# Kernel tuning notes

Hardware: AMD Instinct MI355X
Metric: run time of the kernel (lower is better)

The kernel has to match this reference:

```python
import jax, jax.numpy as jnp
import numpy as np

B, N, D, H, L = 64, 512, 10, 256, 128  # batch, max_size(nodes), node_dim, hidden, latent
AA, SS, ATOM = 20, 7, 5
K = 2  # conv kernel size
L_KLD = 1e-3


def _lin(k, i, o, s=0.02):
    k1, k2 = jax.random.split(k)
    return jax.random.normal(k1, (i, o), jnp.float32) * s, jax.random.normal(k2, (o,), jnp.float32) * s


def setup_inputs() -> dict:
    key = jax.random.key(0)
    ks = iter(jax.random.split(key, 40))
    nk = lambda: next(ks)
    x = jax.random.normal(nk(), (B, N, D), jnp.float32)
    aa = jax.random.randint(nk(), (B, N), 0, AA + 1).astype(jnp.float32)  # 0 = pad -> ignore_idx
    ss = jax.random.randint(nk(), (B, N), 0, SS + 1).astype(jnp.float32)
    x = x.at[:, :, 0].set(aa).at[:, :, 1].set(ss)
    adj = (jax.random.uniform(nk(), (B, N, N)) < 0.1).astype(jnp.float32)  # sparse binary adjacency
    node_mask = jax.random.randint(nk(), (B, N), 0, 2).astype(bool)
    eps = jax.random.uniform(nk(), (B, N, L), jnp.float32)  # torch.rand_like -> uniform
    W_rel, b_rel = _lin(nk(), D, H)
    W_root, _ = _lin(nk(), D, H)  # lin_root has no bias in DenseSAGEConv
    W_mu, b_mu = _lin(nk(), H, L)
    W_lv, b_lv = _lin(nk(), H, L)
    Wx1, bx1 = _lin(nk(), L, 512); Wx2, bx2 = _lin(nk(), 512, 512); Wx3, bx3 = _lin(nk(), 512, H)
    Wa1, ba1 = _lin(nk(), L, 512); Wa2, ba2 = _lin(nk(), 512, 512); Wa3, ba3 = _lin(nk(), 512, H)
    Wc1 = jax.random.normal(nk(), (256, N, K), jnp.float32) * 0.02; bc1 = jnp.zeros((256,), jnp.float32)
    Wc2 = jax.random.normal(nk(), (N, 256, K), jnp.float32) * 0.02; bc2 = jnp.zeros((N,), jnp.float32)
    W_fcx, b_fcx = _lin(nk(), H, AA * SS)
    W_fca, b_fca = _lin(nk(), H, ATOM)
    W_fcj, b_fcj = _lin(nk(), L - 2 * (K - 1), N)  # cnn out len: 128->127->126
    return dict(x=x, adj=adj, node_mask=node_mask, eps=eps, W_rel=W_rel, b_rel=b_rel, W_root=W_root,
                W_mu=W_mu, b_mu=b_mu, W_lv=W_lv, b_lv=b_lv,
                Wx1=Wx1, bx1=bx1, Wx2=Wx2, bx2=bx2, Wx3=Wx3, bx3=bx3,
                Wa1=Wa1, ba1=ba1, Wa2=Wa2, ba2=ba2, Wa3=Wa3, ba3=ba3,
                Wc1=Wc1, bc1=bc1, Wc2=Wc2, bc2=bc2,
                W_fcx=W_fcx, b_fcx=b_fcx, W_fca=W_fca, b_fca=b_fca, W_fcj=W_fcj, b_fcj=b_fcj)


def reference(x, adj, node_mask, eps, W_rel, b_rel, W_root, W_mu, b_mu, W_lv, b_lv,
              Wx1, bx1, Wx2, bx2, Wx3, bx3, Wa1, ba1, Wa2, ba2, Wa3, ba3,
              Wc1, bc1, Wc2, bc2, W_fcx, b_fcx, W_fca, b_fca, W_fcj, b_fcj):
    relu = jax.nn.relu
    # --- encode: DenseSAGEConv(x, adj, mask) ---
    deg = jnp.clip(jnp.sum(adj, axis=-1, keepdims=True), 1.0, None)
    agg = jnp.einsum('bij,bjd->bid', adj, x) / deg           # [B,N,D]
    h = agg @ W_rel + b_rel + x @ W_root                      # [B,N,H]
    h = h * node_mask[..., None].astype(h.dtype)
    h = relu(h)
    mu = h @ W_mu + b_mu
    lv = h @ W_lv + b_lv
    z = mu + eps * jnp.exp(0.5 * lv)                          # [B,N,L]
    # --- decode ---
    hx = relu(relu(z @ Wx1 + bx1) @ Wx2 + bx2) @ Wx3 + bx3    # gen_x MLP
    ha = relu(relu(z @ Wa1 + ba1) @ Wa2 + ba2) @ Wa3 + ba3    # gen_x_atomic MLP
    dn = ('NCH', 'OIH', 'NCH')
    c = relu(jax.lax.conv_general_dilated(z, Wc1, (1,), 'VALID', dimension_numbers=dn) + bc1[None, :, None])
    c = relu(jax.lax.conv_general_dilated(c, Wc2, (1,), 'VALID', dimension_numbers=dn) + bc2[None, :, None])
    out_x_class = hx @ W_fcx + b_fcx                          # [B,N,AA*SS]
    out_x_atom = ha @ W_fca + b_fca                           # [B,N,ATOM]
    out_adj = c @ W_fcj + b_fcj                               # [B,N,126]@[126,N] -> [B,N,N]
    # --- VAE loss (vectorized _input_classes / _binary_adjacency) ---
    mapping = ((x[..., 1] - 1.0) * AA + (x[..., 0] - 1.0)).astype(jnp.int32)  # [B,N]
    valid = mapping >= 0
    logp = jax.nn.log_softmax(out_x_class, axis=-1)
    ce = -jnp.take_along_axis(logp, jnp.clip(mapping, 0)[..., None], axis=-1)[..., 0]
    ce = jnp.mean(jnp.where(valid, ce, 0.0))
    pair = node_mask[:, :, None] & node_mask[:, None, :]
    eye = jnp.eye(adj.shape[1], dtype=bool)[None]
    adj_bin = (pair & (eye | (adj > 0))).astype(out_adj.dtype)
    l = out_adj
    bce = jnp.mean(jnp.maximum(l, 0.0) - l * adj_bin + jnp.log1p(jnp.exp(-jnp.abs(l))))
    mse = jnp.mean((out_x_atom - x[:, :, ATOM:]) ** 2)
    kl = -0.5 * jnp.sum(1.0 + lv - mu ** 2 - jnp.exp(lv))
    sg = jax.lax.stop_gradient
    beta = jnp.abs((sg(ce) + sg(bce)) / sg(mse))
    loss = ce + beta * mse + bce + L_KLD * kl
    return (loss, out_x_class, out_x_atom, out_adj)
```

## Files before the change

### kernel.cpp

```cpp
#include <hip/hip_runtime.h>
#include <hip/hip_bf16.h>
#include <cstdint>

using bf16x8 = __attribute__((ext_vector_type(8))) __bf16;
using floatx4 = __attribute__((ext_vector_type(4))) float;
typedef unsigned short ushort;

#define Nn  512
#define Dd  10
#define Hh  256
#define Ll  128
#define CLS 140
#define ROWS 32768
#define CH  16384

#define OUT_CLASS 1ull
#define OUT_ATOM  4587521ull
#define OUT_ADJ   4751361ull

#define T1_OFF 12ull
#define T2_OFF (12ull + 16777216ull)
#define HX_OFF (12ull + 33554432ull)
#define WT_OFF 41943068ull
#define AXS_OFF 45088780ull
#define Z_OFF  50331644ull

static __device__ __forceinline__ ushort bfb(float v) {
    __hip_bfloat16 h = __float2bfloat16(v);
    return *reinterpret_cast<ushort*>(&h);
}
static __device__ __forceinline__ float fbf(ushort u) {
    __hip_bfloat16 h = *reinterpret_cast<__hip_bfloat16*>(&u);
    return __bfloat162float(h);
}
static __device__ __forceinline__ unsigned pk2(float a, float b) {
    return (unsigned)bfb(a) | ((unsigned)bfb(b) << 16);
}

struct PDesc { const float* src; ushort* dst; int srcR, srcC, Cp, Kp, tile0, mode; };
struct PTable { PDesc d[18]; };

__global__ __launch_bounds__(256) void prep_kernel(PTable tab) {
    __shared__ float tile[32][33];
    int bt = blockIdx.x, tid = threadIdx.x;
    int di = 0;
    #pragma unroll
    for (int i = 1; i < 18; ++i) if (bt >= tab.d[i].tile0) di = i;
    PDesc d = tab.d[di];
    int lt = bt - d.tile0;
    if (d.mode == 1) {
        long base = (long)lt * 8192;
        const float* s = d.src;
        ushort* o = d.dst;
        for (int i = tid; i < 2048; i += 256) {
            long idx = base + (long)i * 4;
            float4 v = *(const float4*)&s[idx];
            unsigned u0 = pk2(v.x, v.y), u1 = pk2(v.z, v.w);
            *(uint2*)&o[idx] = (uint2){u0, u1};
        }
        return;
    }
    int tilesK = (d.Kp + 31) >> 5;
    int k0 = (lt % tilesK) << 5, n0 = (lt / tilesK) << 5;
    int tx = tid & 31, ty = tid >> 5;
    for (int ky = ty; ky < 32; ky += 8) {
        int k = k0 + ky, n = n0 + tx;
        float v = (k < d.srcR && n < d.srcC) ? d.src[(size_t)k * d.srcC + n] : 0.f;
        tile[ky][tx] = v;
    }
    __syncthreads();
    for (int ny = ty; ny < 32; ny += 8) {
        int n = n0 + ny, k = k0 + tx;
        if (n < d.Cp && k < d.Kp) {
            float v = tile[tx][ny];
            if (d.mode >= 64) {
                int koff = d.mode - 64;
                ushort u;
                if (koff >= 32) u = bfb(v - fbf(bfb(v)));
                else u = bfb(v);
                d.dst[(size_t)n * 64 + koff + k] = u;
            } else {
                d.dst[(size_t)n * d.Kp + k] = bfb(v);
            }
        }
    }
}

__global__ __launch_bounds__(256, 8) void agg_kernel(
    const float* __restrict__ adj, const float* __restrict__ x,
    float* __restrict__ axs_g)
{
    __shared__ float4 xs4[1536];
    float* xs = (float*)xs4;
    int tid = threadIdx.x;
    int rowbase = blockIdx.x * 16;
    int b = rowbase >> 9, rowloc = rowbase & 511;
    const float* xb = x + (size_t)b * 5120;
    for (int e = tid; e < 6144; e += 256) {
        int j = e / 12, d = e - j * 12;
        xs[e] = (d < 10) ? xb[j * 10 + d] : 0.f;
    }
    __syncthreads();
    int g = tid >> 4, l16 = tid & 15;
    int row = rowbase + g;
    size_t arow = (size_t)row * Nn;
    float accv[10] = {};
    float deg = 0.f;
    for (int it = 0; it < 32; ++it) {
        int j = l16 + (it << 4);
        float a = adj[arow + j];
        if (a != 0.f) {
            deg += a;
            float4 v0 = xs4[j * 3 + 0];
            float4 v1 = xs4[j * 3 + 1];
            float4 v2 = xs4[j * 3 + 2];
            accv[0] += a * v0.x; accv[1] += a * v0.y;
            accv[2] += a * v0.z; accv[3] += a * v0.w;
            accv[4] += a * v1.x; accv[5] += a * v1.y;
            accv[6] += a * v1.z; accv[7] += a * v1.w;
            accv[8] += a * v2.x; accv[9] += a * v2.y;
        }
    }
    #pragma unroll
    for (int o = 8; o > 0; o >>= 1) {
        deg += __shfl_xor(deg, o);
        #pragma unroll
        for (int d = 0; d < 10; ++d) accv[d] += __shfl_xor(accv[d], o);
    }
    float* orow = axs_g + (size_t)row * 20;
    if (l16 == 0) {
        float dg = fmaxf(deg, 1.f);
        #pragma unroll
        for (int d = 0; d < 10; ++d) orow[d] = accv[d] / dg;
    }
    if (l16 < 10) orow[10 + l16] = xs[(rowloc + g) * 12 + l16];
}

__global__ __launch_bounds__(256, 4) void enc2_kernel(
    const float* __restrict__ axs_g,
    const ushort* __restrict__ Wenc,
    const float* __restrict__ brel, const int* __restrict__ nmask,
    const ushort* __restrict__ Wtmu, const float* __restrict__ bmu,
    const ushort* __restrict__ Wtlv, const float* __restrict__ blv,
    const float* __restrict__ eps, float* __restrict__ Z,
    double* __restrict__ acc_kl)
{
    __shared__ uint4 axsbRaw[160];
    __shared__ uint4 hsbRaw[528];
    __shared__ int smask[16];
    __shared__ float skred[4];
    ushort* axsb = (ushort*)axsbRaw;
    ushort* hsb = (ushort*)hsbRaw;
    int tid = threadIdx.x;
    int rowbase = blockIdx.x * 16;
    size_t abase = (size_t)rowbase * 20;

    for (int e = tid; e < 1280; e += 256) {
        int r = e / 80, d = e - r * 80;
        ushort u = 0;
        if (d < 20) {
            u = bfb(axs_g[abase + r * 20 + d]);
        } else if (d >= 40 && d < 60) {
            float v = axs_g[abase + r * 20 + d - 40];
            u = bfb(v - fbf(bfb(v)));
        }
        axsb[e] = u;
    }
    if (tid < 16) smask[tid] = nmask[rowbase + tid];
    __syncthreads();

    int lane = tid & 63, wid = tid >> 6;
    int l15 = lane & 15, quad = lane >> 4;

    {
        bf16x8 ah = __builtin_bit_cast(bf16x8, *(const uint4*)(axsb + l15 * 80 + quad * 8));
        bf16x8 al = __builtin_bit_cast(bf16x8, *(const uint4*)(axsb + l15 * 80 + 40 + quad * 8));
        #pragma unroll
        for (int i = 0; i < 4; ++i) {
            int ct = wid * 4 + i;
            int col = ct * 16 + l15;
            bf16x8 bh = __builtin_bit_cast(bf16x8, *(const uint4*)(Wenc + (size_t)col * 64 + quad * 8));
            bf16x8 blo = __builtin_bit_cast(bf16x8, *(const uint4*)(Wenc + (size_t)col * 64 + 32 + quad * 8));
            floatx4 a = (floatx4){0.f, 0.f, 0.f, 0.f};
            a = __builtin_amdgcn_mfma_f32_16x16x32_bf16(al, bh, a, 0, 0, 0);
            a = __builtin_amdgcn_mfma_f32_16x16x32_bf16(ah, blo, a, 0, 0, 0);
            a = __builtin_amdgcn_mfma_f32_16x16x32_bf16(ah, bh, a, 0, 0, 0);
            float bb = brel[col];
            #pragma unroll
            for (int r4 = 0; r4 < 4; ++r4) {
                int row = quad * 4 + r4;
                float v = a[r4] + bb;
                v = (smask[row] != 0) ? fmaxf(v, 0.f) : 0.f;
                hsb[row * 264 + col] = bfb(v);
            }
        }
    }
    __syncthreads();

    float kt = 0.f;
    #pragma unroll
    for (int i = 0; i < 2; ++i) {
        int ct = wid * 2 + i;
        int col = ct * 16 + l15;
        floatx4 amu = (floatx4){0.f, 0.f, 0.f, 0.f};
        floatx4 alv = (floatx4){0.f, 0.f, 0.f, 0.f};
        #pragma unroll
        for (int k0 = 0; k0 < 8; ++k0) {
            bf16x8 af = __builtin_bit_cast(bf16x8, *(const uint4*)(hsb + l15 * 264 + k0 * 32 + quad * 8));
            bf16x8 bm = __builtin_bit_cast(bf16x8, *(const uint4*)(Wtmu + (size_t)col * 256 + k0 * 32 + quad * 8));
            bf16x8 bl = __builtin_bit_cast(bf16x8, *(const uint4*)(Wtlv + (size_t)col * 256 + k0 * 32 + quad * 8));
            amu = __builtin_amdgcn_mfma_f32_16x16x32_bf16(af, bm, amu, 0, 0, 0);
            alv = __builtin_amdgcn_mfma_f32_16x16x32_bf16(af, bl, alv, 0, 0, 0);
        }
        float bmv = bmu[col], blv_ = blv[col];
        #pragma unroll
        for (int r4 = 0; r4 < 4; ++r4) {
            int row = quad * 4 + r4;
            size_t zi = ((size_t)rowbase + row) * Ll + col;
            float mu = amu[r4] + bmv;
            float lv = alv[r4] + blv_;
            float ee = eps[zi];
            Z[zi] = mu + ee * expf(0.5f * lv);
            kt += 1.f + lv - mu * mu - expf(lv);
        }
    }
    #pragma unroll
    for (int o = 32; o > 0; o >>= 1) kt += __shfl_xor(kt, o);
    if (lane == 0) skred[wid] = kt;
    __syncthreads();
    if (tid == 0) atomicAdd(acc_kl, (double)(skred[0] + skred[1] + skred[2] + skred[3]));
}

__global__ __launch_bounds__(256) void mgemm_kernel(const void* __restrict__ A, int a_bf16,
                                                    const ushort* __restrict__ Bt,
                                                    const float* __restrict__ bias,
                                                    void* __restrict__ Cp, int c_fp32,
                                                    int N, int K, int ldc, int relu) {
    __shared__ uint4 AsRaw[640];
    __shared__ uint4 BsRaw[640];
    ushort* As = (ushort*)AsRaw;
    ushort* Bs = (ushort*)BsRaw;
    int tid = threadIdx.x;
    int row0 = blockIdx.y << 7, col0 = blockIdx.x << 7;
    int lane = tid & 63, wid = tid >> 6;
    int wm = (wid >> 1) * 64, wn = (wid & 1) * 64;
    int l15 = lane & 15, quad = lane >> 4;
    floatx4 acc[4][4];
    #pragma unroll
    for (int i = 0; i < 4; ++i)
        #pragma unroll
        for (int j = 0; j < 4; ++j) acc[i][j] = (floatx4){0.f, 0.f, 0.f, 0.f};
    int am = tid & 127, aseg = tid >> 7;
    for (int k0 = 0; k0 < K; k0 += 32) {
        {
            uint4* dst = (uint4*)(As + am * 40 + aseg * 16);
            if (a_bf16) {
                const uint4* ap = (const uint4*)((const ushort*)A + (size_t)(row0 + am) * K + k0 + aseg * 16);
                dst[0] = ap[0]; dst[1] = ap[1];
            } else {
                const float4* ap = (const float4*)((const float*)A + (size_t)(row0 + am) * K + k0 + aseg * 16);
                float4 f0 = ap[0], f1 = ap[1], f2 = ap[2], f3 = ap[3];
                dst[0] = (uint4){pk2(f0.x, f0.y), pk2(f0.z, f0.w), pk2(f1.x, f1.y), pk2(f1.z, f1.w)};
                dst[1] = (uint4){pk2(f2.x, f2.y), pk2(f2.z, f2.w), pk2(f3.x, f3.y), pk2(f3.z, f3.w)};
            }
        }
        {
            const uint4* bp = (const uint4*)(Bt + (size_t)(col0 + am) * K + k0 + aseg * 16);
            uint4* dst = (uint4*)(Bs + am * 40 + aseg * 16);
            dst[0] = bp[0]; dst[1] = bp[1];
        }
        __syncthreads();
        bf16x8 af[4], bfv[4];
        #pragma unroll
        for (int mt = 0; mt < 4; ++mt)
            af[mt] = __builtin_bit_cast(bf16x8, *(const uint4*)(As + (wm + mt * 16 + l15) * 40 + quad * 8));
        #pragma unroll
        for (int nt = 0; nt < 4; ++nt)
            bfv[nt] = __builtin_bit_cast(bf16x8, *(const uint4*)(Bs + (wn + nt * 16 + l15) * 40 + quad * 8));
        #pragma unroll
        for (int mt = 0; mt < 4; ++mt)
            #pragma unroll
            for (int nt = 0; nt < 4; ++nt)
                acc[mt][nt] = __builtin_amdgcn_mfma_f32_16x16x32_bf16(af[mt], bfv[nt], acc[mt][nt], 0, 0, 0);
        __syncthreads();
    }
    #pragma unroll
    for (int nt = 0; nt < 4; ++nt) {
        int n = col0 + wn + nt * 16 + l15;
        float bv = bias[n];
        #pragma unroll
        for (int mt = 0; mt < 4; ++mt)
            #pragma unroll
            for (int r = 0; r < 4; ++r) {
                size_t m = row0 + wm + mt * 16 + quad * 4 + r;
                float v = acc[mt][nt][r] + bv;
                if (relu) v = fmaxf(v, 0.f);
                if (c_fp32) ((float*)Cp)[m * ldc + n] = v;
                else ((ushort*)Cp)[m * ldc + n] = bfb(v);
            }
    }
}

__global__ __launch_bounds__(256) void convmfma_kernel(const void* __restrict__ X, int x_bf16,
                                                       long xBS,
                                                       const ushort* __restrict__ Ab,
                                                       const float* __restrict__ bias,
                                                       ushort* __restrict__ Y,
                                                       int Cout, int K, int Tout) {
    __shared__ uint4 AsRaw[640];
    __shared__ uint4 BsRaw[640];
    ushort* As = (ushort*)AsRaw;
    ushort* Bs = (ushort*)BsRaw;
    int tid = threadIdx.x, bz = blockIdx.z;
    int row0 = blockIdx.y << 7;
    int lane = tid & 63, wid = tid >> 6;
    int wm = (wid >> 1) * 64, wn = (wid & 1) * 64;
    int l15 = lane & 15, quad = lane >> 4;
    floatx4 acc[4][4];
    #pragma unroll
    for (int i = 0; i < 4; ++i)
        #pragma unroll
        for (int j = 0; j < 4; ++j) acc[i][j] = (floatx4){0.f, 0.f, 0.f, 0.f};
    int am = tid & 127, aseg = tid >> 7;
    int tnext = (am + 1 > 127) ? 127 : am + 1;
    for (int k0 = 0; k0 < K; k0 += 32) {
        {
            const uint4* ap = (const uint4*)(Ab + (size_t)(row0 + am) * K + k0 + aseg * 16);
            uint4* dst = (uint4*)(As + am * 40 + aseg * 16);
            dst[0] = ap[0]; dst[1] = ap[1];
        }
        {
            unsigned r[8];
            if (x_bf16) {
                const ushort* Xb = (const ushort*)X + (size_t)bz * xBS;
                #pragma unroll
                for (int q = 0; q < 8; ++q) {
                    int kk = k0 + aseg * 16 + 2 * q, i = kk >> 1;
                    r[q] = (unsigned)Xb[i * 128 + am] | ((unsigned)Xb[i * 128 + tnext] << 16);
                }
            } else {
                const float* Xf = (const float*)X + (size_t)bz * xBS;
                #pragma unroll
                for (int q = 0; q < 8; ++q) {
                    int kk = k0 + aseg * 16 + 2 * q, i = kk >> 1;
                    r[q] = pk2(Xf[i * 128 + am], Xf[i * 128 + tnext]);
                }
            }
            uint4* dst = (uint4*)(Bs + am * 40 + aseg * 16);
            dst[0] = (uint4){r[0], r[1], r[2], r[3]};
            dst[1] = (uint4){r[4], r[5], r[6], r[7]};
        }
        __syncthreads();
        bf16x8 af[4], bfv[4];
        #pragma unroll
        for (int mt = 0; mt < 4; ++mt)
            af[mt] = __builtin_bit_cast(bf16x8, *(const uint4*)(As + (wm + mt * 16 + l15) * 40 + quad * 8));
        #pragma unroll
        for (int nt = 0; nt < 4; ++nt)
            bfv[nt] = __builtin_bit_cast(bf16x8, *(const uint4*)(Bs + (wn + nt * 16 + l15) * 40 + quad * 8));
        #pragma unroll
        for (int mt = 0; mt < 4; ++mt)
            #pragma unroll
            for (int nt = 0; nt < 4; ++nt)
                acc[mt][nt] = __builtin_amdgcn_mfma_f32_16x16x32_bf16(af[mt], bfv[nt], acc[mt][nt], 0, 0, 0);
        __syncthreads();
    }
    #pragma unroll
    for (int mt = 0; mt < 4; ++mt)
        #pragma unroll
        for (int r = 0; r < 4; ++r) {
            int m = row0 + wm + mt * 16 + quad * 4 + r;
            float bv = bias[m];
            #pragma unroll
            for (int nt = 0; nt < 4; ++nt) {
                int col = wn + nt * 16 + l15;
                float v = fmaxf(acc[mt][nt][r] + bv, 0.f);
                if (col >= Tout) v = 0.f;
                Y[((size_t)bz * Cout + m) * 128 + col] = bfb(v);
            }
        }
}

__global__ __launch_bounds__(256) void ce_kernel(const ushort* __restrict__ hx,
                                                 const ushort* __restrict__ Wt,
                                                 const float* __restrict__ bfcx,
                                                 const float* __restrict__ x,
                                                 float* __restrict__ out_class,
                                                 double* __restrict__ acc_ce,
                                                 int row0) {
    __shared__ ushort hxb[16 * 264];
    __shared__ float slog[16][144];
    __shared__ float sce[16];
    int tid = threadIdx.x;
    int lbase = blockIdx.x * 16;
    for (int e = tid; e < 512; e += 256) {
        int r = e >> 5, seg = e & 31;
        *(uint4*)(hxb + r * 264 + seg * 8) = *(const uint4*)(hx + (size_t)(lbase + r) * 256 + seg * 8);
    }
    __syncthreads();
    int lane = tid & 63, wid = tid >> 6, l15 = lane & 15, quad = lane >> 4;
    for (int ct = wid; ct < 9; ct += 4) {
        floatx4 a = (floatx4){0.f, 0.f, 0.f, 0.f};
        #pragma unroll
        for (int k0 = 0; k0 < 8; ++k0) {
            bf16x8 af = __builtin_bit_cast(bf16x8, *(const uint4*)(hxb + l15 * 264 + k0 * 32 + quad * 8));
            bf16x8 bfr = __builtin_bit_cast(bf16x8, *(const uint4*)(Wt + (size_t)(ct * 16 + l15) * 256 + k0 * 32 + quad * 8));
            a = __builtin_amdgcn_mfma_f32_16x16x32_bf16(af, bfr, a, 0, 0, 0);
        }
        int col = ct * 16 + l15;
        float bv = (col < CLS) ? bfcx[col] : 0.f;
        #pragma unroll
        for (int r4 = 0; r4 < 4; ++r4) {
            int r = quad * 4 + r4;
            float v = a[r4] + bv;
            slog[r][col] = v;
            if (col < CLS) out_class[(size_t)(row0 + lbase + r) * CLS + col] = v;
        }
    }
    __syncthreads();
    #pragma unroll
    for (int rr = 0; rr < 4; ++rr) {
        int r = wid * 4 + rr;
        float m = -1e30f;
        for (int j = lane; j < CLS; j += 64) m = fmaxf(m, slog[r][j]);
        #pragma unroll
        for (int o = 32; o > 0; o >>= 1) m = fmaxf(m, __shfl_xor(m, o));
        float s = 0.f;
        for (int j = lane; j < CLS; j += 64) s += expf(slog[r][j] - m);
        #pragma unroll
        for (int o = 32; o > 0; o >>= 1) s += __shfl_xor(s, o);
        if (lane == 0) {
            size_t grow = (size_t)row0 + lbase + r;
            float aa = x[grow * Dd + 0];
            float ss = x[grow * Dd + 1];
            int mapping = (int)((ss - 1.f) * 20.f + (aa - 1.f));
            int idx = mapping > 0 ? mapping : 0;
            float ce = -(slog[r][idx] - m - logf(s));
            sce[r] = (mapping < 0) ? 0.f : ce;
        }
    }
    __syncthreads();
    if (tid == 0) {
        float t = 0.f;
        #pragma unroll
        for (int r = 0; r < 16; ++r) t += sce[r];
        atomicAdd(acc_ce, (double)t);
    }
}

__global__ __launch_bounds__(256) void atom_kernel(const ushort* __restrict__ ha,
                                                   const float* __restrict__ Wfca,
                                                   const float* __restrict__ bfca,
                                                   const float* __restrict__ x,
                                                   float* __restrict__ out_atom,
                                                   double* __restrict__ acc_mse,
                                                   int row0) {
    __shared__ double sred[4];
    int tid = threadIdx.x;
    int wid = tid >> 6, lane = tid & 63;
    int rowblk = blockIdx.x * 64;
    double msum = 0.0;
    for (int rr = 0; rr < 16; ++rr) {
        int lrow = rowblk + wid * 16 + rr;
        size_t grow = (size_t)row0 + lrow;
        float acc[5] = {};
        for (int k = lane; k < 256; k += 64) {
            float hv = fbf(ha[(size_t)lrow * Hh + k]);
            #pragma unroll
            for (int o = 0; o < 5; ++o) acc[o] = fmaf(hv, Wfca[k * 5 + o], acc[o]);
        }
        #pragma unroll
        for (int o = 0; o < 5; ++o)
            #pragma unroll
            for (int s = 32; s > 0; s >>= 1) acc[o] += __shfl_xor(acc[o], s);
        if (lane == 0) {
            float ms = 0.f;
            #pragma unroll
            for (int o = 0; o < 5; ++o) {
                float v = acc[o] + bfca[o];
                out_atom[grow * 5 + o] = v;
                float d = v - x[grow * Dd + 5 + o];
                ms += d * d;
            }
            msum += (double)ms;
        }
    }
    if (lane == 0) sred[wid] = msum;
    __syncthreads();
    if (tid == 0) atomicAdd(acc_mse, sred[0] + sred[1] + sred[2] + sred[3]);
}

__global__ __launch_bounds__(256) void bce_kernel(const float* __restrict__ out_adj,
                                                  const float* __restrict__ adj,
                                                  const int* __restrict__ nmask,
                                                  double* __restrict__ acc_bce) {
    __shared__ float sred[4];
    int tid = threadIdx.x;
    float bsum = 0.f;
    for (size_t e = (size_t)blockIdx.x * 256 + tid; e < 16777216ull; e += (size_t)gridDim.x * 256) {
        float l = out_adj[e];
        size_t grow = e >> 9;
        int col = (int)(e & 511);
        int gb = (int)(grow >> 9), n = (int)(grow & 511);
        int mn = nmask[grow];
        int cm = nmask[(size_t)gb * 512 + col];
        float a = adj[e];
        bool abin = (mn != 0) && (cm != 0) && ((col == n) || (a > 0.f));
        bsum += fmaxf(l, 0.f) - (abin ? l : 0.f) + log1pf(expf(-fabsf(l)));
    }
    #pragma unroll
    for (int o = 32; o > 0; o >>= 1) bsum += __shfl_xor(bsum, o);
    if ((tid & 63) == 0) sred[tid >> 6] = bsum;
    __syncthreads();
    if (tid == 0) atomicAdd(acc_bce, (double)(sred[0] + sred[1] + sred[2] + sred[3]));
}

__global__ __launch_bounds__(256) void convgemm_kernel(const float* __restrict__ X,
                                                       const float* __restrict__ Wc,
                                                       const float* __restrict__ bias,
                                                       float* __restrict__ Y,
                                                       int Cin, int Tin, int Cout) {
    __shared__ float As[16][68];
    __shared__ float Bs[16][68];
    int K = Cin * 2, Tout = Tin - 1;
    int tid = threadIdx.x, bz = blockIdx.z;
    const float* Xb = X + (size_t)bz * Cin * Tin;
    int m0 = blockIdx.y << 6, col0 = blockIdx.x << 6;
    int tx = tid & 15, ty = tid >> 4;
    float acc[4][4] = {};
    int sm = tid & 63, sks = (tid >> 6) << 2;
    int bkk = tid >> 4, btof = (tid & 15) << 2;
    for (int k0 = 0; k0 < K; k0 += 16) {
        float4 av = *(const float4*)&Wc[(size_t)(m0 + sm) * K + k0 + sks];
        As[sks + 0][sm] = av.x; As[sks + 1][sm] = av.y;
        As[sks + 2][sm] = av.z; As[sks + 3][sm] = av.w;
        {
            int kg = k0 + bkk, i = kg >> 1, par = kg & 1;
            const float* xr = Xb + (size_t)i * Tin;
            #pragma unroll
            for (int j = 0; j < 4; ++j) {
                int t = col0 + btof + j + par;
                if (t > Tin - 1) t = Tin - 1;
                Bs[bkk][btof + j] = xr[t];
            }
        }
        __syncthreads();
        #pragma unroll
        for (int kk = 0; kk < 16; ++kk) {
            float4 a4 = *(const float4*)&As[kk][ty << 2];
            float4 b4 = *(const float4*)&Bs[kk][tx << 2];
            float a[4] = {a4.x, a4.y, a4.z, a4.w};
            float bb[4] = {b4.x, b4.y, b4.z, b4.w};
            #pragma unroll
            for (int i = 0; i < 4; ++i)
                #pragma unroll
                for (int j = 0; j < 4; ++j)
                    acc[i][j] = fmaf(a[i], bb[j], acc[i][j]);
        }
        __syncthreads();
    }
    #pragma unroll
    for (int i = 0; i < 4; ++i) {
        int m = m0 + (ty << 2) + i;
        float bv = bias[m];
        #pragma unroll
        for (int j = 0; j < 4; ++j) {
            int col = col0 + (tx << 2) + j;
            if (col < Tout)
                Y[((size_t)bz * Cout + m) * Tout + col] = fmaxf(acc[i][j] + bv, 0.f);
        }
    }
}

__global__ __launch_bounds__(256) void adjbce_kernel(const float* __restrict__ c2,
                                                     const float* __restrict__ Wfcj,
                                                     const float* __restrict__ bfcj,
                                                     const float* __restrict__ adj,
                                                     const int* __restrict__ nmask,
                                                     float* __restrict__ out_adj,
                                                     double* __restrict__ acc_bce,
                                                     int b0) {
    __shared__ float cs[8][126];
    __shared__ int smn[8];
    __shared__ float sred[4];
    int tid = threadIdx.x;
    int lbase = blockIdx.x * 8;
    size_t growbase = (size_t)b0 * Nn + lbase;
    int gb = (int)(growbase >> 9);
    for (int e = tid; e < 8 * 126; e += 256) {
        int r = e / 126, k = e - r * 126;
        cs[r][k] = c2[(size_t)(lbase + r) * 126 + k];
    }
    if (tid < 8) smn[tid] = nmask[growbase + tid];
    __syncthreads();
    int j0 = tid, j1 = tid + 256;
    float l0[8], l1[8];
    float bj0 = bfcj[j0], bj1 = bfcj[j1];
    #pragma unroll
    for (int r = 0; r < 8; ++r) { l0[r] = bj0; l1[r] = bj1; }
    for (int k = 0; k < 126; ++k) {
        float w0 = Wfcj[k * Nn + j0];
        float w1 = Wfcj[k * Nn + j1];
        #pragma unroll
        for (int r = 0; r < 8; ++r) {
            float cv = cs[r][k];
            l0[r] = fmaf(cv, w0, l0[r]);
            l1[r] = fmaf(cv, w1, l1[r]);
        }
    }
    int cm0 = nmask[(size_t)(gb << 9) + j0];
    int cm1 = nmask[(size_t)(gb << 9) + j1];
    float bsum = 0.f;
    #pragma unroll
    for (int r = 0; r < 8; ++r) {
        size_t grow = growbase + r;
        int n = (int)(grow & 511);
        int mn = smn[r];
        float a0 = adj[grow * Nn + j0];
        float a1 = adj[grow * Nn + j1];
        out_adj[grow * Nn + j0] = l0[r];
        out_adj[grow * Nn + j1] = l1[r];
        bool ab0 = (mn != 0) && (cm0 != 0) && ((j0 == n) || (a0 > 0.f));
        bool ab1 = (mn != 0) && (cm1 != 0) && ((j1 == n) || (a1 > 0.f));
        bsum += fmaxf(l0[r], 0.f) - (ab0 ? l0[r] : 0.f) + log1pf(expf(-fabsf(l0[r])));
        bsum += fmaxf(l1[r], 0.f) - (ab1 ? l1[r] : 0.f) + log1pf(expf(-fabsf(l1[r])));
    }
    #pragma unroll
    for (int o = 32; o > 0; o >>= 1) bsum += __shfl_xor(bsum, o);
    if ((tid & 63) == 0) sred[tid >> 6] = bsum;
    __syncthreads();
    if (tid == 0) atomicAdd(acc_bce, (double)(sred[0] + sred[1] + sred[2] + sred[3]));
}

__global__ void loss_kernel(const double* __restrict__ acc, float* __restrict__ out) {
    double ce  = acc[0] / 32768.0;
    double bce = acc[1] / 16777216.0;
    double mse = acc[2] / 163840.0;
    double kl  = -0.5 * acc[3];
    double bm = (mse != 0.0) ? fabs(ce + bce) : 0.0;
    out[0] = (float)(ce + bm + bce + 1e-3 * kl);
}

extern "C" void kernel_launch(void* const* d_in, const int* in_sizes, int n_in,
                              void* d_out, int out_size, void* d_ws, size_t ws_size,
                              hipStream_t stream) {
    const float* x      = (const float*)d_in[0];
    const float* adj    = (const float*)d_in[1];
    const int*   nmask  = (const int*)d_in[2];
    const float* eps    = (const float*)d_in[3];
    const float* W_rel  = (const float*)d_in[4];
    const float* b_rel  = (const float*)d_in[5];
    const float* W_root = (const float*)d_in[6];
    const float* W_mu   = (const float*)d_in[7];
    const float* b_mu   = (const float*)d_in[8];
    const float* W_lv   = (const float*)d_in[9];
    const float* b_lv   = (const float*)d_in[10];
    const float* Wx1    = (const float*)d_in[11];
    const float* bx1    = (const float*)d_in[12];
    const float* Wx2    = (const float*)d_in[13];
    const float* bx2    = (const float*)d_in[14];
    const float* Wx3    = (const float*)d_in[15];
    const float* bx3    = (const float*)d_in[16];
    const float* Wa1    = (const float*)d_in[17];
    const float* ba1    = (const float*)d_in[18];
    const float* Wa2    = (const float*)d_in[19];
    const float* ba2    = (const float*)d_in[20];
    const float* Wa3    = (const float*)d_in[21];
    const float* ba3    = (const float*)d_in[22];
    const float* Wc1    = (const float*)d_in[23];
    const float* bc1    = (const float*)d_in[24];
    const float* Wc2    = (const float*)d_in[25];
    const float* bc2    = (const float*)d_in[26];
    const float* W_fcx  = (const float*)d_in[27];
    const float* b_fcx  = (const float*)d_in[28];
    const float* W_fca  = (const float*)d_in[29];
    const float* b_fca  = (const float*)d_in[30];
    const float* W_fcj  = (const float*)d_in[31];
    const float* b_fcj  = (const float*)d_in[32];

    float* out = (float*)d_out;
    char* region = (char*)(out + OUT_ADJ);
    ushort* t1 = (ushort*)(region + T1_OFF);
    ushort* t2 = (ushort*)(region + T2_OFF);
    ushort* hx = (ushort*)(region + HX_OFF);
    float*  Z  = (float*)(region + Z_OFF);
    float*  axs_g = (float*)(region + AXS_OFF);

    ushort* wt_x1  = (ushort*)(region + WT_OFF);
    ushort* wt_x2  = wt_x1 + 65536;
    ushort* wt_x3  = wt_x2 + 262144;
    ushort* wt_a1  = wt_x3 + 131072;
    ushort* wt_a2  = wt_a1 + 65536;
    ushort* wt_a3  = wt_a2 + 262144;
    ushort* wt_mu  = wt_a3 + 131072;
    ushort* wt_lv  = wt_mu + 32768;
    ushort* wt_fcx = wt_lv + 32768;
    ushort* wt_enc = wt_fcx + 36864;

    double* acc = (double*)d_ws;
    ushort* wc1b   = (ushort*)((char*)d_ws + 256);
    ushort* wc2b   = wc1b + 262144;
    ushort* wt_fcj = wc2b + 262144;
    char* convbuf = (char*)d_ws + 1179904;
    bool fastConv = ws_size >= (size_t)1179904 + 196608;

    hipMemsetAsync(d_ws, 0, 256, stream);

    PTable tab;
    int t0 = 0;
    auto setT = [&](int i, const float* s, ushort* d, int R, int C, int Cp, int Kp) {
        tab.d[i] = {s, d, R, C, Cp, Kp, t0, 0};
        t0 += ((Cp + 31) / 32) * ((Kp + 31) / 32);
    };
    setT(0, Wx1, wt_x1, 128, 512, 512, 128);
    setT(1, Wx2, wt_x2, 512, 512, 512, 512);
    setT(2, Wx3, wt_x3, 512, 256, 256, 512);
    setT(3, Wa1, wt_a1, 128, 512, 512, 128);
    setT(4, Wa2, wt_a2, 512, 512, 512, 512);
    setT(5, Wa3, wt_a3, 512, 256, 256, 512);
    setT(6, W_mu, wt_mu, 256, 128, 128, 256);
    setT(7, W_lv, wt_lv, 256, 128, 128, 256);
    setT(8,  W_rel,  wt_enc, 10, 256, 256, 10); tab.d[8].mode  = 64 + 0;
    setT(9,  W_root, wt_enc, 10, 256, 256, 10); tab.d[9].mode  = 64 + 10;
    setT(10, W_rel,  wt_enc, 0,  0,   256, 12); tab.d[10].mode = 64 + 20;
    setT(11, W_rel,  wt_enc, 10, 256, 256, 10); tab.d[11].mode = 64 + 32;
    setT(12, W_root, wt_enc, 10, 256, 256, 10); tab.d[12].mode = 64 + 42;
    setT(13, W_rel,  wt_enc, 0,  0,   256, 12); tab.d[13].mode = 64 + 52;
    setT(14, W_fcx, wt_fcx, 256, 140, 144, 256);
    int t_nofcj = t0;
    setT(15, W_fcj, wt_fcj, 126, 512, 512, 128);
    tab.d[16] = {Wc1, wc1b, 262144, 0, 0, 0, t0, 1}; t0 += 32;
    tab.d[17] = {Wc2, wc2b, 262144, 0, 0, 0, t0, 1}; t0 += 32;
    prep_kernel<<<fastConv ? t0 : t_nofcj, 256, 0, stream>>>(tab);

    agg_kernel<<<ROWS / 16, 256, 0, stream>>>(adj, x, axs_g);
    enc2_kernel<<<ROWS / 16, 256, 0, stream>>>(axs_g, wt_enc, b_rel, nmask,
                                               wt_mu, b_mu, wt_lv, b_lv, eps, Z, acc + 3);

    for (int c = 0; c < 2; ++c) {
        int r0 = c * CH;
        mgemm_kernel<<<dim3(4, 128), 256, 0, stream>>>(Z + (size_t)r0 * Ll, 0, wt_x1, bx1, t1, 0, 512, 128, 512, 1);
        mgemm_kernel<<<dim3(4, 128), 256, 0, stream>>>(t1, 1, wt_x2, bx2, t2, 0, 512, 512, 512, 1);
        mgemm_kernel<<<dim3(2, 128), 256, 0, stream>>>(t2, 1, wt_x3, bx3, hx, 0, 256, 512, 256, 0);
        ce_kernel<<<CH / 16, 256, 0, stream>>>(hx, wt_fcx, b_fcx, x, out + OUT_CLASS, acc + 0, r0);
    }
    for (int c = 0; c < 2; ++c) {
        int r0 = c * CH;
        mgemm_kernel<<<dim3(4, 128), 256, 0, stream>>>(Z + (size_t)r0 * Ll, 0, wt_a1, ba1, t1, 0, 512, 128, 512, 1);
        mgemm_kernel<<<dim3(4, 128), 256, 0, stream>>>(t1, 1, wt_a2, ba2, t2, 0, 512, 512, 512, 1);
        mgemm_kernel<<<dim3(2, 128), 256, 0, stream>>>(t2, 1, wt_a3, ba3, hx, 0, 256, 512, 256, 0);
        atom_kernel<<<CH / 64, 256, 0, stream>>>(hx, W_fca, b_fca, x, out + OUT_ATOM, acc + 2, r0);
    }

    if (fastConv) {
        size_t avail = ws_size - 1179904;
        int NB = 64;
        while (NB > 1 && (size_t)NB * 196608 > avail) NB >>= 1;
        ushort* c1 = (ushort*)convbuf;
        ushort* c2 = c1 + (size_t)NB * 32768;
        for (int b0 = 0; b0 < 64; b0 += NB) {
            convmfma_kernel<<<dim3(1, 2, NB), 256, 0, stream>>>(Z + (size_t)b0 * 65536, 0, 65536,
                                                               wc1b, bc1, c1, 256, 1024, 127);
            convmfma_kernel<<<dim3(1, 4, NB), 256, 0, stream>>>(c1, 1, 32768,
                                                               wc2b, bc2, c2, 512, 512, 126);
            mgemm_kernel<<<dim3(4, NB * 4), 256, 0, stream>>>(c2, 1, wt_fcj, b_fcj,
                                                              out + OUT_ADJ + (size_t)b0 * 262144, 1,
                                                              512, 128, 512, 0);
        }
        bce_kernel<<<1024, 256, 0, stream>>>(out + OUT_ADJ, adj, nmask, acc + 1);
    } else {
        size_t avail = (ws_size > 256) ? ws_size - 256 : 0;
        int NB = 64;
        while (NB > 1 && (size_t)NB * 388096 > avail) NB >>= 1;
        float* c1 = (float*)((char*)d_ws + 256);
        float* c2 = (float*)((char*)d_ws + 256 + (size_t)NB * 256 * 127 * 4);
        for (int b0 = 0; b0 < 64; b0 += NB) {
            convgemm_kernel<<<dim3(2, 4, NB), 256, 0, stream>>>(Z + (size_t)b0 * 65536, Wc1, bc1, c1, 512, 128, 256);
            convgemm_kernel<<<dim3(2, 8, NB), 256, 0, stream>>>(c1, Wc2, bc2, c2, 256, 127, 512);
            adjbce_kernel<<<NB * Nn / 8, 256, 0, stream>>>(c2, W_fcj, b_fcj, adj, nmask,
                                                           out + OUT_ADJ, acc + 1, b0);
        }
    }

    loss_kernel<<<1, 1, 0, stream>>>(acc, out);
}
```

Before: 877.3 us.

## Pack adjacency into bitmask during aggregation and use it in BCE reduction

The aggregation kernel, which already streams the dense fp32 adjacency, now writes a per-row bitmask of nonzero entries using wave ballots. The BCE kernel reads this compact bitmask instead of re-reading the 64 MB adjacency. It also processes row blocks with cached node-mask values and uses fast __logf/__expf intrinsics. Separately, the GEMM epilogue loop order is swapped so stores iterate over rows outermost. The extra bitmask writes add a little traffic to the aggregation pass and require more workspace.

Result: faster. 816.6 us (-6.9%).

```diff
diff --git a/kernel.cpp b/kernel.cpp
--- a/kernel.cpp
+++ b/kernel.cpp
@@ -23,6 +23,7 @@
 #define HX_OFF (12ull + 33554432ull)
 #define WT_OFF 41943068ull
 #define AXS_OFF 45088780ull
+#define ABITS_FB_OFF 47710224ull
 #define Z_OFF  50331644ull
 
 static __device__ __forceinline__ ushort bfb(float v) {
@@ -88,7 +89,7 @@
 
 __global__ __launch_bounds__(256, 8) void agg_kernel(
     const float* __restrict__ adj, const float* __restrict__ x,
-    float* __restrict__ axs_g)
+    float* __restrict__ axs_g, ushort* __restrict__ abits)
 {
     __shared__ float4 xs4[1536];
     float* xs = (float*)xs4;
@@ -109,6 +110,8 @@
     for (int it = 0; it < 32; ++it) {
         int j = l16 + (it << 4);
         float a = adj[arow + j];
+        unsigned long long bal = __ballot(a > 0.f);
+        if (l16 == 0) abits[(size_t)row * 32 + it] = (ushort)(bal >> ((g & 3) << 4));
         if (a != 0.f) {
             deg += a;
             float4 v0 = xs4[j * 3 + 0];
@@ -284,21 +287,27 @@
                 acc[mt][nt] = __builtin_amdgcn_mfma_f32_16x16x32_bf16(af[mt], bfv[nt], acc[mt][nt], 0, 0, 0);
         __syncthreads();
     }
+    float bvv[4];
+    int ncols[4];
     #pragma unroll
     for (int nt = 0; nt < 4; ++nt) {
-        int n = col0 + wn + nt * 16 + l15;
-        float bv = bias[n];
-        #pragma unroll
-        for (int mt = 0; mt < 4; ++mt)
-            #pragma unroll
-            for (int r = 0; r < 4; ++r) {
-                size_t m = row0 + wm + mt * 16 + quad * 4 + r;
-                float v = acc[mt][nt][r] + bv;
+        ncols[nt] = col0 + wn + nt * 16 + l15;
+        bvv[nt] = bias[ncols[nt]];
+    }
+    #pragma unroll
+    for (int mt = 0; mt < 4; ++mt)
+        #pragma unroll
+        for (int r = 0; r < 4; ++r) {
+            size_t m = row0 + wm + mt * 16 + quad * 4 + r;
+            #pragma unroll
+            for (int nt = 0; nt < 4; ++nt) {
+                int n = ncols[nt];
+                float v = acc[mt][nt][r] + bvv[nt];
                 if (relu) v = fmaxf(v, 0.f);
                 if (c_fp32) ((float*)Cp)[m * ldc + n] = v;
                 else ((ushort*)Cp)[m * ldc + n] = bfb(v);
             }
-    }
+        }
 }
 
 __global__ __launch_bounds__(256) void convmfma_kernel(const void* __restrict__ X, int x_bf16,
@@ -490,23 +499,36 @@
     if (tid == 0) atomicAdd(acc_mse, sred[0] + sred[1] + sred[2] + sred[3]);
 }
 
-__global__ __launch_bounds__(256) void bce_kernel(const float* __restrict__ out_adj,
-                                                  const float* __restrict__ adj,
-                                                  const int* __restrict__ nmask,
-                                                  double* __restrict__ acc_bce) {
+__global__ __launch_bounds__(256) void bce2_kernel(const float* __restrict__ out_adj,
+                                                   const ushort* __restrict__ abits,
+                                                   const int* __restrict__ nmask,
+                                                   double* __restrict__ acc_bce) {
+    __shared__ int smn[32];
     __shared__ float sred[4];
     int tid = threadIdx.x;
+    int rowbase = blockIdx.x * 32;
+    int gb = rowbase >> 9;
+    if (tid < 32) smn[tid] = nmask[rowbase + tid];
+    int j0 = tid, j1 = tid + 256;
+    int cm0 = nmask[gb * 512 + j0];
+    int cm1 = nmask[gb * 512 + j1];
+    __syncthreads();
+    int l15 = tid & 15;
     float bsum = 0.f;
-    for (size_t e = (size_t)blockIdx.x * 256 + tid; e < 16777216ull; e += (size_t)gridDim.x * 256) {
-        float l = out_adj[e];
-        size_t grow = e >> 9;
-        int col = (int)(e & 511);
-        int gb = (int)(grow >> 9), n = (int)(grow & 511);
-        int mn = nmask[grow];
-        int cm = nmask[(size_t)gb * 512 + col];
-        float a = adj[e];
-        bool abin = (mn != 0) && (cm != 0) && ((col == n) || (a > 0.f));
-        bsum += fmaxf(l, 0.f) - (abin ? l : 0.f) + log1pf(expf(-fabsf(l)));
+    for (int r = 0; r < 32; ++r) {
+        size_t grow = (size_t)(rowbase + r);
+        int n = (int)(grow & 511);
+        int mn = smn[r];
+        const float* lrow = out_adj + grow * 512;
+        const ushort* wrow = abits + grow * 32;
+        float l0 = lrow[j0];
+        float l1 = lrow[j1];
+        int b0 = (wrow[j0 >> 4] >> l15) & 1;
+        int b1 = (wrow[j1 >> 4] >> l15) & 1;
+        bool ab0 = (mn != 0) && (cm0 != 0) && ((j0 == n) || b0);
+        bool ab1 = (mn != 0) && (cm1 != 0) && ((j1 == n) || b1);
+        bsum += fmaxf(l0, 0.f) - (ab0 ? l0 : 0.f) + __logf(1.f + __expf(-fabsf(l0)));
+        bsum += fmaxf(l1, 0.f) - (ab1 ? l1 : 0.f) + __logf(1.f + __expf(-fabsf(l1)));
     }
     #pragma unroll
     for (int o = 32; o > 0; o >>= 1) bsum += __shfl_xor(bsum, o);
@@ -701,8 +723,10 @@
     ushort* wc1b   = (ushort*)((char*)d_ws + 256);
     ushort* wc2b   = wc1b + 262144;
     ushort* wt_fcj = wc2b + 262144;
-    char* convbuf = (char*)d_ws + 1179904;
-    bool fastConv = ws_size >= (size_t)1179904 + 196608;
+    ushort* abits_ws = (ushort*)((char*)d_ws + 1179904);
+    char* convbuf = (char*)d_ws + 1179904 + 2097152;
+    bool fastConv = ws_size >= (size_t)1179904 + 2097152 + 196608;
+    ushort* abits = fastConv ? abits_ws : (ushort*)(region + ABITS_FB_OFF);
 
     hipMemsetAsync(d_ws, 0, 256, stream);
 
@@ -733,7 +757,7 @@
     tab.d[17] = {Wc2, wc2b, 262144, 0, 0, 0, t0, 1}; t0 += 32;
     prep_kernel<<<fastConv ? t0 : t_nofcj, 256, 0, stream>>>(tab);
 
-    agg_kernel<<<ROWS / 16, 256, 0, stream>>>(adj, x, axs_g);
+    agg_kernel<<<ROWS / 16, 256, 0, stream>>>(adj, x, axs_g, abits);
     enc2_kernel<<<ROWS / 16, 256, 0, stream>>>(axs_g, wt_enc, b_rel, nmask,
                                                wt_mu, b_mu, wt_lv, b_lv, eps, Z, acc + 3);
 
@@ -753,7 +777,7 @@
     }
 
     if (fastConv) {
-        size_t avail = ws_size - 1179904;
+        size_t avail = ws_size - 1179904 - 2097152;
         int NB = 64;
         while (NB > 1 && (size_t)NB * 196608 > avail) NB >>= 1;
         ushort* c1 = (ushort*)convbuf;
@@ -767,7 +791,7 @@
                                                               out + OUT_ADJ + (size_t)b0 * 262144, 1,
                                                               512, 128, 512, 0);
         }
-        bce_kernel<<<1024, 256, 0, stream>>>(out + OUT_ADJ, adj, nmask, acc + 1);
+        bce2_kernel<<<1024, 256, 0, stream>>>(out + OUT_ADJ, abits, nmask, acc + 1);
     } else {
         size_t avail = (ws_size > 256) ? ws_size - 256 : 0;
         int NB = 64;
```
